# Kernel optimization log

Measured on AMD Instinct MI355X. Metric: run time of the kernel, lower is better.

The kernel has to match this reference:

```python
import jax, jax.numpy as jnp
import numpy as np

KERNEL_NUM = 16
KERNEL_SIZE = 3

def setup_inputs() -> dict:
    key = jax.random.key(0)
    k1, k2 = jax.random.split(key)
    x = jax.random.normal(k1, (32, 512, 512), dtype=jnp.float32)
    # nn.init.normal_(kernels, mean=0, std=1/kernel_size**2)
    kernels = jax.random.normal(k2, (KERNEL_NUM, KERNEL_SIZE, KERNEL_SIZE), dtype=jnp.float32) / (KERNEL_SIZE ** 2)
    return {"x": x, "kernels": kernels}

def reference(x, kernels):
    # valid, stride-1, single-channel 2D conv (cross-correlation, as in the torch einsum)
    # x: [B, H, W] -> [B, 1, H, W]; kernels: [K, kh, kw] -> [K, 1, kh, kw]
    lhs = x[:, None, :, :]
    rhs = kernels[:, None, :, :]
    out = jax.lax.conv_general_dilated(
        lhs, rhs,
        window_strides=(1, 1),
        padding="VALID",
        dimension_numbers=("NCHW", "OIHW", "NCHW"),
    )
    return out  # [B, K, H-kh+1, W-kw+1]
```

## Files before the change

kernel.cpp:

```cpp
#include <hip/hip_runtime.h>

#define IH 512
#define IW 512
#define OH 510
#define OW 510
#define NB 32
#define KO 16
#define OHW (OH * OW)
#define PPB 8
#define LO 1020

typedef float f32x4 __attribute__((ext_vector_type(4)));
typedef float f32x2 __attribute__((ext_vector_type(2)));

__global__ __launch_bounds__(256, 4) void conv3x3_k16_kernel(
    const float* __restrict__ x,
    const float* __restrict__ k,
    float* __restrict__ out)
{
    __shared__ float lds[PPB * LO];

    const int bid  = blockIdx.x;
    const int oh   = bid & 1;
    const int tile = bid >> 1;
    const int n  = tile / (OH / 2);
    const int i0 = (tile - n * (OH / 2)) * 2;
    const int t  = threadIdx.x;
    const int half = t >> 7;
    const int tt = t & 127;
    const int i  = i0 + half;
    const bool tail = (tt == 127);

    int j;
    if ((i & 1) == 0) j = tail ? 508 : 4 * tt;
    else              j = tail ? 0   : 4 * tt + 2;

    const float* xr = x + ((size_t)n * IH + i) * IW + j;

    float xv[3][6];
#pragma unroll
    for (int r = 0; r < 3; ++r) {
        const float2 a = *reinterpret_cast<const float2*>(xr + r * IW);
        const float2 b = *reinterpret_cast<const float2*>(xr + r * IW + 2);
        xv[r][0] = a.x; xv[r][1] = a.y; xv[r][2] = b.x; xv[r][3] = b.y;
        if (!tail) {
            const float2 c = *reinterpret_cast<const float2*>(xr + r * IW + 4);
            xv[r][4] = c.x; xv[r][5] = c.y;
        } else {
            xv[r][4] = 0.0f; xv[r][5] = 0.0f;
        }
    }

    const int lbase = half * OW + j;
#pragma unroll
    for (int ol = 0; ol < PPB; ++ol) {
        const int o = PPB * oh + ol;
        float a0 = 0.f, a1 = 0.f, a2 = 0.f, a3 = 0.f;
#pragma unroll
        for (int r = 0; r < 3; ++r)
#pragma unroll
            for (int c = 0; c < 3; ++c) {
                const float kv = k[(o * 3 + r) * 3 + c];
                a0 = fmaf(xv[r][c],     kv, a0);
                a1 = fmaf(xv[r][c + 1], kv, a1);
                a2 = fmaf(xv[r][c + 2], kv, a2);
                a3 = fmaf(xv[r][c + 3], kv, a3);
            }
        float* lp = &lds[ol * LO + lbase];
        f32x2 v0; v0[0] = a0; v0[1] = a1;
        *reinterpret_cast<f32x2*>(lp) = v0;
        if (!tail) {
            f32x2 v1; v1[0] = a2; v1[1] = a3;
            *reinterpret_cast<f32x2*>(lp + 2) = v1;
        }
    }

    __syncthreads();

    if (t < 255) {
        float* ob = out + (((size_t)(n * KO + PPB * oh)) * OH + i0) * OW;
        const int f = 4 * t;
#pragma unroll
        for (int ol = 0; ol < PPB; ++ol) {
            const f32x4 v = *reinterpret_cast<const f32x4*>(&lds[ol * LO + f]);
            __builtin_nontemporal_store(v,
                reinterpret_cast<f32x4*>(ob + (size_t)ol * OHW + f));
        }
    }
}

extern "C" void kernel_launch(void* const* d_in, const int* in_sizes, int n_in,
                              void* d_out, int out_size, void* d_ws, size_t ws_size,
                              hipStream_t stream) {
    const float* x   = (const float*)d_in[0];
    const float* ker = (const float*)d_in[1];
    float* out       = (float*)d_out;

    dim3 grid(NB * (OH / 2) * 2);
    dim3 block(256);
    conv3x3_k16_kernel<<<grid, block, 0, stream>>>(x, ker, out);
}
```

Before: 121.6 us.

## Make blocks persistent over row bands with double-buffered LDS staging

Each block now walks a band of 15 row-pairs instead of handling a single row-pair. It double-buffers the LDS output staging and prefetches the next row's inputs into registers while the current tile drains to global memory. The goal is to overlap loads, FMAs and stores within a block and to cut the number of launched blocks. In exchange, occupancy drops (launch bounds go to 2 and LDS use doubles), fewer blocks run (32*17*2 = 1088), and a single barrier per stage with alternating buffers relies on tight ordering to avoid a WAR race on buffer reuse.

```diff
diff --git a/kernel.cpp b/kernel.cpp
--- a/kernel.cpp
+++ b/kernel.cpp
@@ -9,52 +9,38 @@
 #define OHW (OH * OW)
 #define PPB 8
 #define LO 1020
+#define TQ 15
+#define NBAND 17
 
 typedef float f32x4 __attribute__((ext_vector_type(4)));
 typedef float f32x2 __attribute__((ext_vector_type(2)));
 
-__global__ __launch_bounds__(256, 4) void conv3x3_k16_kernel(
-    const float* __restrict__ x,
-    const float* __restrict__ k,
-    float* __restrict__ out)
+
+__device__ __forceinline__ void load_xv(const float* __restrict__ xr,
+                                        bool tail, float v[3][6])
 {
-    __shared__ float lds[PPB * LO];
-
-    const int bid  = blockIdx.x;
-    const int oh   = bid & 1;
-    const int tile = bid >> 1;
-    const int n  = tile / (OH / 2);
-    const int i0 = (tile - n * (OH / 2)) * 2;
-    const int t  = threadIdx.x;
-    const int half = t >> 7;
-    const int tt = t & 127;
-    const int i  = i0 + half;
-    const bool tail = (tt == 127);
-
-    int j;
-    if ((i & 1) == 0) j = tail ? 508 : 4 * tt;
-    else              j = tail ? 0   : 4 * tt + 2;
-
-    const float* xr = x + ((size_t)n * IH + i) * IW + j;
-
-    float xv[3][6];
 #pragma unroll
     for (int r = 0; r < 3; ++r) {
         const float2 a = *reinterpret_cast<const float2*>(xr + r * IW);
         const float2 b = *reinterpret_cast<const float2*>(xr + r * IW + 2);
-        xv[r][0] = a.x; xv[r][1] = a.y; xv[r][2] = b.x; xv[r][3] = b.y;
+        v[r][0] = a.x; v[r][1] = a.y; v[r][2] = b.x; v[r][3] = b.y;
         if (!tail) {
             const float2 c = *reinterpret_cast<const float2*>(xr + r * IW + 4);
-            xv[r][4] = c.x; xv[r][5] = c.y;
+            v[r][4] = c.x; v[r][5] = c.y;
         } else {
-            xv[r][4] = 0.0f; xv[r][5] = 0.0f;
+            v[r][4] = 0.0f; v[r][5] = 0.0f;
         }
     }
+}
 
-    const int lbase = half * OW + j;
+__device__ __forceinline__ void fma_to_lds(const float xv[3][6],
+                                           const float* __restrict__ k,
+                                           int ob, float* __restrict__ buf,
+                                           int lbase, bool tail)
+{
 #pragma unroll
     for (int ol = 0; ol < PPB; ++ol) {
-        const int o = PPB * oh + ol;
+        const int o = ob + ol;
         float a0 = 0.f, a1 = 0.f, a2 = 0.f, a3 = 0.f;
 #pragma unroll
         for (int r = 0; r < 3; ++r)
@@ -66,7 +52,7 @@
                 a2 = fmaf(xv[r][c + 2], kv, a2);
                 a3 = fmaf(xv[r][c + 3], kv, a3);
             }
-        float* lp = &lds[ol * LO + lbase];
+        float* lp = buf + ol * LO + lbase;
         f32x2 v0; v0[0] = a0; v0[1] = a1;
         *reinterpret_cast<f32x2*>(lp) = v0;
         if (!tail) {
@@ -74,17 +60,88 @@
             *reinterpret_cast<f32x2*>(lp + 2) = v1;
         }
     }
+}
 
-    __syncthreads();
+__device__ __forceinline__ void drain_tile(const float* __restrict__ buf,
+                                           float* __restrict__ ob, int f,
+                                           bool active)
+{
+    if (active) {
+        f32x4 s0 = *reinterpret_cast<const f32x4*>(buf + 0 * LO + f);
+        f32x4 s1 = *reinterpret_cast<const f32x4*>(buf + 1 * LO + f);
+        f32x4 s2 = *reinterpret_cast<const f32x4*>(buf + 2 * LO + f);
+        f32x4 s3 = *reinterpret_cast<const f32x4*>(buf + 3 * LO + f);
+        f32x4 s4 = *reinterpret_cast<const f32x4*>(buf + 4 * LO + f);
+        f32x4 s5 = *reinterpret_cast<const f32x4*>(buf + 5 * LO + f);
+        f32x4 s6 = *reinterpret_cast<const f32x4*>(buf + 6 * LO + f);
+        f32x4 s7 = *reinterpret_cast<const f32x4*>(buf + 7 * LO + f);
+        __builtin_nontemporal_store(s0, reinterpret_cast<f32x4*>(ob + (size_t)0 * OHW + f));
+        __builtin_nontemporal_store(s1, reinterpret_cast<f32x4*>(ob + (size_t)1 * OHW + f));
+        __builtin_nontemporal_store(s2, reinterpret_cast<f32x4*>(ob + (size_t)2 * OHW + f));
+        __builtin_nontemporal_store(s3, reinterpret_cast<f32x4*>(ob + (size_t)3 * OHW + f));
+        __builtin_nontemporal_store(s4, reinterpret_cast<f32x4*>(ob + (size_t)4 * OHW + f));
+        __builtin_nontemporal_store(s5, reinterpret_cast<f32x4*>(ob + (size_t)5 * OHW + f));
+        __builtin_nontemporal_store(s6, reinterpret_cast<f32x4*>(ob + (size_t)6 * OHW + f));
+        __builtin_nontemporal_store(s7, reinterpret_cast<f32x4*>(ob + (size_t)7 * OHW + f));
+    }
+}
 
-    if (t < 255) {
-        float* ob = out + (((size_t)(n * KO + PPB * oh)) * OH + i0) * OW;
-        const int f = 4 * t;
-#pragma unroll
-        for (int ol = 0; ol < PPB; ++ol) {
-            const f32x4 v = *reinterpret_cast<const f32x4*>(&lds[ol * LO + f]);
-            __builtin_nontemporal_store(v,
-                reinterpret_cast<f32x4*>(ob + (size_t)ol * OHW + f));
+__global__ __launch_bounds__(256, 2) void conv3x3_k16_kernel(
+    const float* __restrict__ x,
+    const float* __restrict__ k,
+    float* __restrict__ out)
+{
+    __shared__ float lds[2][PPB * LO];
+
+    const int bid  = blockIdx.x;
+    const int oh   = bid & 1;
+    const int rest = bid >> 1;
+    const int band = rest % NBAND;
+    const int n    = rest / NBAND;
+    const int rp0  = band * TQ;
+
+    const int t    = threadIdx.x;
+    const int half = t >> 7;
+    const int tt   = t & 127;
+    const bool tail = (tt == 127);
+    const int ob_f = PPB * oh;
+
+    int j;
+    if (half == 0) j = tail ? 508 : 4 * tt;
+    else           j = tail ? 0   : 4 * tt + 2;
+    const int lbase = half * OW + j;
+    const int f = 4 * t;
+    const bool active = (t < 255);
+
+    const float* xn = x + (size_t)n * IH * IW;
+    float* on = out + ((size_t)(n * KO + ob_f)) * OHW;
+
+    float xvA[3][6], xvB[3][6];
+    load_xv(xn + (size_t)(2 * rp0 + half) * IW + j, tail, xvA);
+
+#pragma unroll 1
+    for (int q = 0; q < TQ; q += 2) {
+        {
+            const int rp = rp0 + q;
+            fma_to_lds(xvA, k, ob_f, &lds[0][0], lbase, tail);
+            const int rpn = (q + 1 < TQ) ? rp + 1 : rp;
+            load_xv(xn + (size_t)(2 * rpn + half) * IW + j, tail, xvB);
+            asm volatile("s_waitcnt lgkmcnt(0)" ::: "memory");
+            __builtin_amdgcn_sched_barrier(0);
+            __builtin_amdgcn_s_barrier();
+            __builtin_amdgcn_sched_barrier(0);
+            drain_tile(&lds[0][0], on + (size_t)(2 * rp) * OW, f, active);
+        }
+        if (q + 1 < TQ) {
+            const int rp = rp0 + q + 1;
+            fma_to_lds(xvB, k, ob_f, &lds[1][0], lbase, tail);
+            const int rpn = (q + 2 < TQ) ? rp + 1 : rp;
+            load_xv(xn + (size_t)(2 * rpn + half) * IW + j, tail, xvA);
+            asm volatile("s_waitcnt lgkmcnt(0)" ::: "memory");
+            __builtin_amdgcn_sched_barrier(0);
+            __builtin_amdgcn_s_barrier();
+            __builtin_amdgcn_sched_barrier(0);
+            drain_tile(&lds[1][0], on + (size_t)(2 * rp) * OW, f, active);
         }
     }
 }
@@ -96,7 +153,7 @@
     const float* ker = (const float*)d_in[1];
     float* out       = (float*)d_out;
 
-    dim3 grid(NB * (OH / 2) * 2);
+    dim3 grid(NB * NBAND * 2);
     dim3 block(256);
     conv3x3_k16_kernel<<<grid, block, 0, stream>>>(x, ker, out);
 }
```

After: 160.9 us. 32.3% more time.
